# Optimization experiments

Hardware: AMD Instinct MI355X
Metric: run time of the kernel (lower is better)

## Reference

```python
import jax, jax.numpy as jnp
import numpy as np

N, C, DIM, K = 1024, 8, 128, 3
LBP_LOOPS = 10
DAMP = 0.5


def setup_inputs() -> dict:
    key = jax.random.key(0)
    ks = jax.random.split(key, 6)
    return {
        "E": jax.random.normal(ks[0], (N, C, DIM), dtype=jnp.float32),   # candidate entity embeddings e_{i,c}
        "F": jax.random.normal(ks[1], (N, DIM), dtype=jnp.float32),      # mention reps f(m_i) (f_m_c output)
        "Fc": jax.random.normal(ks[2], (N, DIM), dtype=jnp.float32),     # context reps f(c_i)
        "B": jax.random.normal(ks[3], (DIM,), dtype=jnp.float32),        # diagonal of B
        "R": jax.random.normal(ks[4], (K, DIM), dtype=jnp.float32),      # diagonals of R[k]
        "D": jax.random.normal(ks[5], (K, DIM), dtype=jnp.float32),      # diagonals of D[k]
    }


def reference(E, F, Fc, B, R, D):
    n, c, d = E.shape
    # psi[i, ci] = e_{i,ci}^T diag(B) f(c_i)
    psi = jnp.einsum('icd,d,id->ic', E, B, Fc)
    # a[i,j,k] = softmax_k( f_i^T diag(D[k]) f_j / sqrt(d) )   (RelNorm Z)
    logits = jnp.einsum('id,kd,jd->ijk', F, D, F) / jnp.sqrt(jnp.asarray(d, E.dtype))
    a = jax.nn.softmax(logits, axis=-1)
    # phi[i,j,ci,cj] = sum_k a[i,j,k] * e_{i,ci}^T diag(R[k]) e_{j,cj}
    Rw = jnp.einsum('ijk,kd->ijd', a, R)                 # [n, n, d]
    phi = jnp.einsum('icd,ijd,jed->ijce', E, Rw, E)      # [n, n, C, C]

    def lbp_step(mbar, _):
        # mbar[src, dst, cand_of_dst]
        incoming = mbar.sum(axis=0)                                 # [i, ci]
        excl = incoming[:, None, :] - jnp.transpose(mbar, (1, 0, 2))  # [i, j, ci] = sum_{k != j} mbar[k,i,ci]
        score = psi[:, None, :, None] + excl[:, :, :, None] + phi   # [i, j, ci, cj]
        msg = score.max(axis=2)                                     # max over ci -> [i, j, cj]
        new = jnp.log(DAMP * jax.nn.softmax(msg, axis=-1) + (1.0 - DAMP) * jnp.exp(mbar))
        return new, None

    mbar0 = jnp.zeros((n, n, c), dtype=E.dtype)
    mbar, _ = jax.lax.scan(lbp_step, mbar0, None, length=LBP_LOOPS)

    # ubar[i,c] = softmax_c( psi[i,c] + sum_{k != i} mbar[k,i,c] )
    self_msg = mbar[jnp.arange(n), jnp.arange(n)]        # [n, C]
    u = psi + mbar.sum(axis=0) - self_msg
    return jax.nn.softmax(u, axis=-1)
```

## Files before the change

kernel.cpp:

```cpp
#include <hip/hip_runtime.h>
#include <math.h>

#define N 1024
#define C 8
#define DIM 128
#define K 3
#define LBP_LOOPS 10
#define DAMP 0.5f

#define TI 16
#define TJ 16
#define DCH 32
#define ESTR 260
#define FSTR 132
#define SR 136
#define NT 64
#define NTILE 2080

typedef float v4f __attribute__((ext_vector_type(4)));

__device__ __forceinline__ int tri_base(int t) { return t * NT - (t * (t - 1)) / 2; }
__device__ __forceinline__ void tri_decode(int b, int& ti, int& tj) {
    int t = (int)((2.f * NT + 1.f - sqrtf((2.f * NT + 1.f) * (2.f * NT + 1.f) - 8.f * (float)b)) * 0.5f);
    t = min(max(t, 0), NT - 1);
    while (tri_base(t) > b) --t;
    while (tri_base(t + 1) <= b) ++t;
    ti = t; tj = t + (b - tri_base(t));
}

__device__ __forceinline__ size_t tri_idx(int i, int j) {
    return (size_t)i * N - (((size_t)i * (i - 1)) >> 1) + (size_t)(j - i);
}

__global__ void psi_kernel(const float* __restrict__ E, const float* __restrict__ Fc,
                           const float* __restrict__ B, float* __restrict__ psi) {
    int x = blockIdx.x * blockDim.x + threadIdx.x;
    if (x >= N * C) return;
    int i = x / C;
    const float* e = E + (size_t)x * DIM;
    const float* fc = Fc + (size_t)i * DIM;
    float s = 0.f;
#pragma unroll 8
    for (int d = 0; d < DIM; ++d) s = fmaf(e[d] * B[d], fc[d], s);
    psi[x] = s;
}


__global__ __launch_bounds__(256, 2) void phi_i16_sym_kernel(
    const float* __restrict__ E, const float* __restrict__ F,
    const float* __restrict__ R, const float* __restrict__ D,
    short* __restrict__ phiQ, float* __restrict__ pscale)
{
    __shared__ __align__(16) float sU[2 * TI * ESTR];
    int ti, tj;
    tri_decode(blockIdx.x, ti, tj);
    int i0 = ti * 16, j0 = tj * 16;
    int tid = threadIdx.x;
    int il = tid >> 4, jl = tid & 15;

    float* sFi = sU;
    float* sFj = sU + TI * FSTR;
    float* sEi = sU;
    float* sEj = sU + TI * ESTR;

    {
        const v4f* F4 = (const v4f*)F;
        for (int t = tid; t < TI * DIM / 4; t += 256) {
            int r = t >> 5, d4 = t & 31;
            *(v4f*)&sFi[r * FSTR + d4 * 4] = F4[(size_t)(i0 + r) * (DIM / 4) + d4];
            *(v4f*)&sFj[r * FSTR + d4 * 4] = F4[(size_t)(j0 + r) * (DIM / 4) + d4];
        }
    }
    __syncthreads();

    v4f lga0 = {0.f,0.f,0.f,0.f}, lga1 = lga0, lga2 = lga0;
    {
        const v4f* D4 = (const v4f*)D;
#pragma unroll 8
        for (int d4 = 0; d4 < DIM / 4; ++d4) {
            v4f fi = *(const v4f*)&sFi[il * FSTR + d4 * 4];
            v4f fj = *(const v4f*)&sFj[jl * FSTR + d4 * 4];
            v4f ff = fi * fj;
            lga0 += ff * D4[d4];
            lga1 += ff * D4[DIM / 4 + d4];
            lga2 += ff * D4[2 * DIM / 4 + d4];
        }
    }
    float lg0 = lga0.x + lga0.y + lga0.z + lga0.w;
    float lg1 = lga1.x + lga1.y + lga1.z + lga1.w;
    float lg2 = lga2.x + lga2.y + lga2.z + lga2.w;
    const float scale = 0.088388347648318447f;
    lg0 *= scale; lg1 *= scale; lg2 *= scale;
    float mx = fmaxf(fmaxf(lg0, lg1), lg2);
    float e0 = __expf(lg0 - mx), e1 = __expf(lg1 - mx), e2 = __expf(lg2 - mx);
    float inv = 1.f / (e0 + e1 + e2);
    float a0 = e0 * inv, a1 = e1 * inv, a2 = e2 * inv;

    float acc[C][C];
#pragma unroll
    for (int ci = 0; ci < C; ++ci)
#pragma unroll
        for (int cj = 0; cj < C; ++cj) acc[ci][cj] = 0.f;

    const v4f* R4 = (const v4f*)R;
    for (int d0 = 0; d0 < DIM; d0 += DCH) {
        __syncthreads();
        for (int t = tid; t < TI * C * DCH; t += 256) {
            int loc = t >> 8, ci = (t >> 5) & 7, d = t & 31;
            sEi[loc * ESTR + ci * DCH + d] = E[((size_t)(i0 + loc) * C + ci) * DIM + d0 + d];
            sEj[loc * ESTR + ci * DCH + d] = E[((size_t)(j0 + loc) * C + ci) * DIM + d0 + d];
        }
        __syncthreads();
#pragma unroll
        for (int d4 = 0; d4 < DCH / 4; ++d4) {
            int rq = (d0 >> 2) + d4;
            v4f rw = R4[rq] * a0 + R4[(DIM >> 2) + rq] * a1 + R4[(DIM >> 1) + rq] * a2;
            v4f ei[C];
#pragma unroll
            for (int ci = 0; ci < C; ++ci)
                ei[ci] = *(const v4f*)&sEi[il * ESTR + ci * DCH + d4 * 4] * rw;
#pragma unroll
            for (int cj = 0; cj < C; ++cj) {
                v4f ej = *(const v4f*)&sEj[jl * ESTR + cj * DCH + d4 * 4];
#pragma unroll
                for (int ci = 0; ci < C; ++ci) {
                    acc[ci][cj] = fmaf(ei[ci].x, ej.x, acc[ci][cj]);
                    acc[ci][cj] = fmaf(ei[ci].y, ej.y, acc[ci][cj]);
                    acc[ci][cj] = fmaf(ei[ci].z, ej.z, acc[ci][cj]);
                    acc[ci][cj] = fmaf(ei[ci].w, ej.w, acc[ci][cj]);
                }
            }
        }
    }

    int i = i0 + il, j = j0 + jl;
    if (i > j) return;

    float amax = 0.f;
#pragma unroll
    for (int ci = 0; ci < C; ++ci)
#pragma unroll
        for (int cj = 0; cj < C; ++cj) amax = fmaxf(amax, fabsf(acc[ci][cj]));
    float qs = (amax > 0.f) ? (32767.0f / amax) : 1.0f;

    size_t tri = tri_idx(i, j);
    pscale[tri] = (amax > 0.f) ? (amax / 32767.0f) : 0.f;

    int4* out = (int4*)(phiQ + tri * (C * C));
#pragma unroll
    for (int ci = 0; ci < C; ++ci) {
        int q[C];
#pragma unroll
        for (int cj = 0; cj < C; ++cj) q[cj] = (int)rintf(acc[ci][cj] * qs);
        int4 v;
        v.x = (q[0] & 0xFFFF) | (q[1] << 16);
        v.y = (q[2] & 0xFFFF) | (q[3] << 16);
        v.z = (q[4] & 0xFFFF) | (q[5] << 16);
        v.w = (q[6] & 0xFFFF) | (q[7] << 16);
        out[ci] = v;
    }
}


__device__ __forceinline__ void damp_calc(const float msg[C], const float mpv[C], float o[C]) {
    float mx = msg[0];
#pragma unroll
    for (int c = 1; c < C; ++c) mx = fmaxf(mx, msg[c]);
    float e[C], s = 0.f;
#pragma unroll
    for (int c = 0; c < C; ++c) { e[c] = __expf(msg[c] - mx); s += e[c]; }
    float inv = DAMP / s;
#pragma unroll
    for (int c = 0; c < C; ++c)
        o[c] = __logf(fmaf(e[c], inv, (1.f - DAMP) * __expf(mpv[c])));
}

template <bool FIRST>
__global__ __launch_bounds__(256) void lbp_tile(
    const short* __restrict__ phiQ, const float* __restrict__ pscale,
    const float* __restrict__ mprev, float* __restrict__ mnext,
    const float* __restrict__ incpsi, float* __restrict__ partInc)
{
    int ti, tj;
    tri_decode(blockIdx.x, ti, tj);
    bool diag = (ti == tj);
    __shared__ __align__(16) float sA[16 * SR];
    __shared__ __align__(16) float sB[16 * SR];
    __shared__ float sInc[256];
    int tid = threadIdx.x;
    int i0 = ti * 16, j0 = tj * 16;

    if (!FIRST) {
        const float4* __restrict__ src = (const float4*)mprev;
        for (int t = tid; t < 512; t += 256) {
            int row = t >> 5, rem = t & 31;
            float4 v = src[((size_t)(i0 + row) * N + j0) * 2 + rem];
            *(float4*)&sA[row * SR + rem * 4] = v;
        }
        if (!diag) {
            for (int t = tid; t < 512; t += 256) {
                int row = t >> 5, rem = t & 31;
                float4 v = src[((size_t)(j0 + row) * N + i0) * 2 + rem];
                *(float4*)&sB[row * SR + rem * 4] = v;
            }
        }
    }
    if (tid < 128) sInc[tid] = incpsi[i0 * C + tid];
    else sInc[tid] = incpsi[j0 * C + (tid - 128)];
    __syncthreads();

    int il = tid >> 4, jl = tid & 15;
    int i = i0 + il, j = j0 + jl;
    bool active = (!diag) || (jl >= il);
    bool dopair = active && (j > i);
    const float* sBB = diag ? sA : sB;

    float out_ij[C], out_ji[C];
    if (active) {
        float mij[C], mji[C], sci[C], scj[C];
#pragma unroll
        for (int c = 0; c < C; ++c) {
            mij[c] = FIRST ? 0.f : sA[il * SR + jl * 8 + c];
            mji[c] = FIRST ? 0.f : sBB[jl * SR + il * 8 + c];
            sci[c] = sInc[il * 8 + c] - mji[c];
            scj[c] = sInc[128 + jl * 8 + c] - mij[c];
        }

        size_t tri = tri_idx(i, j);
        float s = pscale[tri];
        float msg_ij[C], msg_ji[C];
#pragma unroll
        for (int c = 0; c < C; ++c) { msg_ij[c] = -1e30f; msg_ji[c] = -1e30f; }

        const int4* p4 = (const int4*)(phiQ + tri * (C * C));
#pragma unroll
        for (int ci = 0; ci < C; ++ci) {
            int4 v = p4[ci];
            float ph[C];
            ph[0] = (float)((int)(short)(v.x & 0xFFFF)) * s;
            ph[1] = (float)(v.x >> 16) * s;
            ph[2] = (float)((int)(short)(v.y & 0xFFFF)) * s;
            ph[3] = (float)(v.y >> 16) * s;
            ph[4] = (float)((int)(short)(v.z & 0xFFFF)) * s;
            ph[5] = (float)(v.z >> 16) * s;
            ph[6] = (float)((int)(short)(v.w & 0xFFFF)) * s;
            ph[7] = (float)(v.w >> 16) * s;
#pragma unroll
            for (int cj = 0; cj < C; ++cj) {
                msg_ij[cj] = fmaxf(msg_ij[cj], sci[ci] + ph[cj]);
                msg_ji[ci] = fmaxf(msg_ji[ci], scj[cj] + ph[cj]);
            }
        }
        damp_calc(msg_ij, mij, out_ij);
        if (dopair) damp_calc(msg_ji, mji, out_ji);
    }
    __syncthreads();

    if (active) {
#pragma unroll
        for (int c = 0; c < C; ++c) sA[il * SR + jl * 8 + c] = out_ij[c];
        if (dopair) {
            if (diag) {
#pragma unroll
                for (int c = 0; c < C; ++c) sA[jl * SR + il * 8 + c] = out_ji[c];
            } else {
#pragma unroll
                for (int c = 0; c < C; ++c) sB[jl * SR + il * 8 + c] = out_ji[c];
            }
        }
    }
    __syncthreads();

    {
        float4* __restrict__ dst = (float4*)mnext;
        for (int t = tid; t < 512; t += 256) {
            int row = t >> 5, rem = t & 31;
            dst[((size_t)(i0 + row) * N + j0) * 2 + rem] = *(const float4*)&sA[row * SR + rem * 4];
        }
        if (!diag) {
            for (int t = tid; t < 512; t += 256) {
                int row = t >> 5, rem = t & 31;
                dst[((size_t)(j0 + row) * N + i0) * 2 + rem] = *(const float4*)&sB[row * SR + rem * 4];
            }
        }
    }

    if (tid < 128) {
        int l = tid >> 3, c = tid & 7;
        float s = 0.f;
#pragma unroll
        for (int k = 0; k < 16; ++k) s += sA[k * SR + l * 8 + c];
        partInc[(size_t)ti * (N * C) + (j0 + l) * C + c] = s;
    } else if (!diag) {
        int t2 = tid - 128;
        int l = t2 >> 3, c = t2 & 7;
        float s = 0.f;
#pragma unroll
        for (int k = 0; k < 16; ++k) s += sB[k * SR + l * 8 + c];
        partInc[(size_t)tj * (N * C) + (i0 + l) * C + c] = s;
    }
}

__global__ void incfin_kernel(const float* __restrict__ partInc, const float* __restrict__ psi,
                              float* __restrict__ incpsi) {
    int x = blockIdx.x * 256 + threadIdx.x;
    if (x >= N * C) return;
    float s = psi[x];
#pragma unroll 8
    for (int g = 0; g < NT; ++g) s += partInc[(size_t)g * (N * C) + x];
    incpsi[x] = s;
}

__global__ void final_kernel(const float* __restrict__ incpsi, const float* __restrict__ mbar,
                             float* __restrict__ out) {
    int i = blockIdx.x * blockDim.x + threadIdx.x;
    if (i >= N) return;
    float u[C];
    float mx = -1e30f;
#pragma unroll
    for (int c = 0; c < C; ++c) {
        u[c] = incpsi[i * C + c] - mbar[((size_t)i * N + i) * C + c];
        mx = fmaxf(mx, u[c]);
    }
    float s = 0.f;
#pragma unroll
    for (int c = 0; c < C; ++c) { u[c] = __expf(u[c] - mx); s += u[c]; }
    float inv = 1.f / s;
#pragma unroll
    for (int c = 0; c < C; ++c) out[i * C + c] = u[c] * inv;
}


extern "C" void kernel_launch(void* const* d_in, const int* in_sizes, int n_in,
                              void* d_out, int out_size, void* d_ws, size_t ws_size,
                              hipStream_t stream) {
    const float* E  = (const float*)d_in[0];
    const float* F  = (const float*)d_in[1];
    const float* Fc = (const float*)d_in[2];
    const float* B  = (const float*)d_in[3];
    const float* R  = (const float*)d_in[4];
    const float* D  = (const float*)d_in[5];
    float* out = (float*)d_out;

    const size_t NPAIR   = (size_t)N * (N + 1) / 2;
    const size_t PHI_SZ  = NPAIR * C * C * 2;
    const size_t PSC_SZ  = NPAIR * 4;
    const size_t MBAR    = (size_t)N * N * C * 4;
    const size_t PART_SZ = (size_t)NT * N * C * 4;

    char* p = (char*)d_ws;
    short* phiQ   = (short*)p;                     p += PHI_SZ;
    float* pscale = (float*)p;                     p += PSC_SZ;
    float* mbar0  = (float*)p;                     p += MBAR;
    float* mbar1  = (float*)p;                     p += MBAR;
    float* partInc= (float*)p;                     p += PART_SZ;
    float* psi    = (float*)p;                     p += (size_t)N * C * 4;
    float* incpsi = (float*)p;

    psi_kernel<<<dim3((N * C + 255) / 256), 256, 0, stream>>>(E, Fc, B, psi);
    phi_i16_sym_kernel<<<dim3(NTILE), 256, 0, stream>>>(E, F, R, D, phiQ, pscale);

    float* cur = mbar0;
    float* nxt = mbar1;
    lbp_tile<true><<<dim3(NTILE), 256, 0, stream>>>(phiQ, pscale, cur, nxt, psi, partInc);
    incfin_kernel<<<dim3((N * C + 255) / 256), 256, 0, stream>>>(partInc, psi, incpsi);
    { float* t = cur; cur = nxt; nxt = t; }
    for (int it = 1; it < LBP_LOOPS; ++it) {
        lbp_tile<false><<<dim3(NTILE), 256, 0, stream>>>(phiQ, pscale, cur, nxt, incpsi, partInc);
        incfin_kernel<<<dim3((N * C + 255) / 256), 256, 0, stream>>>(partInc, psi, incpsi);
        float* t = cur; cur = nxt; nxt = t;
    }
    final_kernel<<<dim3((N + 255) / 256), 256, 0, stream>>>(incpsi, cur, out);
}
```

Before: 476.9 us.

## Prefetch E chunks into registers with vectorized loads to overlap phi compute

```diff
diff --git a/kernel.cpp b/kernel.cpp
--- a/kernel.cpp
+++ b/kernel.cpp
@@ -11,8 +11,10 @@
 #define TI 16
 #define TJ 16
 #define DCH 32
+#define NCH (DIM / DCH)
 #define ESTR 260
 #define FSTR 132
+#define SIDE (TI * ESTR)
 #define SR 136
 #define NT 64
 #define NTILE 2080
@@ -51,20 +53,21 @@
     const float* __restrict__ R, const float* __restrict__ D,
     short* __restrict__ phiQ, float* __restrict__ pscale)
 {
-    __shared__ __align__(16) float sU[2 * TI * ESTR];
+    __shared__ __align__(16) float sU[2 * SIDE];
     int ti, tj;
     tri_decode(blockIdx.x, ti, tj);
     int i0 = ti * 16, j0 = tj * 16;
     int tid = threadIdx.x;
     int il = tid >> 4, jl = tid & 15;
 
-    float* sFi = sU;
-    float* sFj = sU + TI * FSTR;
-    float* sEi = sU;
-    float* sEj = sU + TI * ESTR;
+    const v4f* E4 = (const v4f*)E;
+    const v4f* F4 = (const v4f*)F;
+    const v4f* R4 = (const v4f*)R;
+    const v4f* D4 = (const v4f*)D;
 
     {
-        const v4f* F4 = (const v4f*)F;
+        float* sFi = sU;
+        float* sFj = sU + TI * FSTR;
         for (int t = tid; t < TI * DIM / 4; t += 256) {
             int r = t >> 5, d4 = t & 31;
             *(v4f*)&sFi[r * FSTR + d4 * 4] = F4[(size_t)(i0 + r) * (DIM / 4) + d4];
@@ -73,9 +76,32 @@
     }
     __syncthreads();
 
-    v4f lga0 = {0.f,0.f,0.f,0.f}, lga1 = lga0, lga2 = lga0;
+    int q0 = tid, q1 = tid + 256, q2 = tid + 512, q3 = tid + 768;
+    int loc0 = q0 >> 6, ci0 = (q0 >> 3) & 7, dd0 = q0 & 7;
+    int loc1 = q1 >> 6, ci1 = (q1 >> 3) & 7, dd1 = q1 & 7;
+    int loc2 = q2 >> 6, ci2 = (q2 >> 3) & 7, dd2 = q2 & 7;
+    int loc3 = q3 >> 6, ci3 = (q3 >> 3) & 7, dd3 = q3 & 7;
+    size_t gi0 = ((size_t)(i0 + loc0) * C + ci0) * (DIM / 4) + dd0;
+    size_t gi1 = ((size_t)(i0 + loc1) * C + ci1) * (DIM / 4) + dd1;
+    size_t gi2 = ((size_t)(i0 + loc2) * C + ci2) * (DIM / 4) + dd2;
+    size_t gi3 = ((size_t)(i0 + loc3) * C + ci3) * (DIM / 4) + dd3;
+    size_t gj0 = ((size_t)(j0 + loc0) * C + ci0) * (DIM / 4) + dd0;
+    size_t gj1 = ((size_t)(j0 + loc1) * C + ci1) * (DIM / 4) + dd1;
+    size_t gj2 = ((size_t)(j0 + loc2) * C + ci2) * (DIM / 4) + dd2;
+    size_t gj3 = ((size_t)(j0 + loc3) * C + ci3) * (DIM / 4) + dd3;
+    int l0 = loc0 * ESTR + ci0 * DCH + dd0 * 4;
+    int l1 = loc1 * ESTR + ci1 * DCH + dd1 * 4;
+    int l2 = loc2 * ESTR + ci2 * DCH + dd2 * 4;
+    int l3 = loc3 * ESTR + ci3 * DCH + dd3 * 4;
+
+    v4f rA0 = E4[gi0], rA1 = E4[gi1], rA2 = E4[gi2], rA3 = E4[gi3];
+    v4f rB0 = E4[gj0], rB1 = E4[gj1], rB2 = E4[gj2], rB3 = E4[gj3];
+
+    float a0, a1, a2;
     {
-        const v4f* D4 = (const v4f*)D;
+        const float* sFi = sU;
+        const float* sFj = sU + TI * FSTR;
+        v4f lga0 = {0.f,0.f,0.f,0.f}, lga1 = lga0, lga2 = lga0;
 #pragma unroll 8
         for (int d4 = 0; d4 < DIM / 4; ++d4) {
             v4f fi = *(const v4f*)&sFi[il * FSTR + d4 * 4];
@@ -85,16 +111,23 @@
             lga1 += ff * D4[DIM / 4 + d4];
             lga2 += ff * D4[2 * DIM / 4 + d4];
         }
-    }
-    float lg0 = lga0.x + lga0.y + lga0.z + lga0.w;
-    float lg1 = lga1.x + lga1.y + lga1.z + lga1.w;
-    float lg2 = lga2.x + lga2.y + lga2.z + lga2.w;
-    const float scale = 0.088388347648318447f;
-    lg0 *= scale; lg1 *= scale; lg2 *= scale;
-    float mx = fmaxf(fmaxf(lg0, lg1), lg2);
-    float e0 = __expf(lg0 - mx), e1 = __expf(lg1 - mx), e2 = __expf(lg2 - mx);
-    float inv = 1.f / (e0 + e1 + e2);
-    float a0 = e0 * inv, a1 = e1 * inv, a2 = e2 * inv;
+        float lg0 = lga0.x + lga0.y + lga0.z + lga0.w;
+        float lg1 = lga1.x + lga1.y + lga1.z + lga1.w;
+        float lg2 = lga2.x + lga2.y + lga2.z + lga2.w;
+        const float scale = 0.088388347648318447f;
+        lg0 *= scale; lg1 *= scale; lg2 *= scale;
+        float mx = fmaxf(fmaxf(lg0, lg1), lg2);
+        float e0 = __expf(lg0 - mx), e1 = __expf(lg1 - mx), e2 = __expf(lg2 - mx);
+        float inv = 1.f / (e0 + e1 + e2);
+        a0 = e0 * inv; a1 = e1 * inv; a2 = e2 * inv;
+    }
+    __syncthreads();
+
+    *(v4f*)&sU[l0] = rA0; *(v4f*)&sU[l1] = rA1;
+    *(v4f*)&sU[l2] = rA2; *(v4f*)&sU[l3] = rA3;
+    *(v4f*)&sU[SIDE + l0] = rB0; *(v4f*)&sU[SIDE + l1] = rB1;
+    *(v4f*)&sU[SIDE + l2] = rB2; *(v4f*)&sU[SIDE + l3] = rB3;
+    __syncthreads();
 
     float acc[C][C];
 #pragma unroll
@@ -102,26 +135,27 @@
 #pragma unroll
         for (int cj = 0; cj < C; ++cj) acc[ci][cj] = 0.f;
 
-    const v4f* R4 = (const v4f*)R;
-    for (int d0 = 0; d0 < DIM; d0 += DCH) {
-        __syncthreads();
-        for (int t = tid; t < TI * C * DCH; t += 256) {
-            int loc = t >> 8, ci = (t >> 5) & 7, d = t & 31;
-            sEi[loc * ESTR + ci * DCH + d] = E[((size_t)(i0 + loc) * C + ci) * DIM + d0 + d];
-            sEj[loc * ESTR + ci * DCH + d] = E[((size_t)(j0 + loc) * C + ci) * DIM + d0 + d];
-        }
-        __syncthreads();
+    for (int c = 0; c < NCH; ++c) {
+        if (c < NCH - 1) {
+            size_t off = (size_t)((c + 1) * (DCH / 4));
+            rA0 = E4[gi0 + off]; rA1 = E4[gi1 + off];
+            rA2 = E4[gi2 + off]; rA3 = E4[gi3 + off];
+            rB0 = E4[gj0 + off]; rB1 = E4[gj1 + off];
+            rB2 = E4[gj2 + off]; rB3 = E4[gj3 + off];
+        }
+        const float* bi = sU + il * ESTR;
+        const float* bj = sU + SIDE + jl * ESTR;
 #pragma unroll
         for (int d4 = 0; d4 < DCH / 4; ++d4) {
-            int rq = (d0 >> 2) + d4;
-            v4f rw = R4[rq] * a0 + R4[(DIM >> 2) + rq] * a1 + R4[(DIM >> 1) + rq] * a2;
+            int rq = c * (DCH / 4) + d4;
+            v4f rw = R4[rq] * a0 + R4[(DIM / 4) + rq] * a1 + R4[(DIM / 2) + rq] * a2;
             v4f ei[C];
 #pragma unroll
             for (int ci = 0; ci < C; ++ci)
-                ei[ci] = *(const v4f*)&sEi[il * ESTR + ci * DCH + d4 * 4] * rw;
+                ei[ci] = *(const v4f*)&bi[ci * DCH + d4 * 4] * rw;
 #pragma unroll
             for (int cj = 0; cj < C; ++cj) {
-                v4f ej = *(const v4f*)&sEj[jl * ESTR + cj * DCH + d4 * 4];
+                v4f ej = *(const v4f*)&bj[cj * DCH + d4 * 4];
 #pragma unroll
                 for (int ci = 0; ci < C; ++ci) {
                     acc[ci][cj] = fmaf(ei[ci].x, ej.x, acc[ci][cj]);
@@ -130,6 +164,14 @@
                     acc[ci][cj] = fmaf(ei[ci].w, ej.w, acc[ci][cj]);
                 }
             }
+        }
+        if (c < NCH - 1) {
+            __syncthreads();
+            *(v4f*)&sU[l0] = rA0; *(v4f*)&sU[l1] = rA1;
+            *(v4f*)&sU[l2] = rA2; *(v4f*)&sU[l3] = rA3;
+            *(v4f*)&sU[SIDE + l0] = rB0; *(v4f*)&sU[SIDE + l1] = rB1;
+            *(v4f*)&sU[SIDE + l2] = rB2; *(v4f*)&sU[SIDE + l3] = rB3;
+            __syncthreads();
         }
     }
 
```

Result: slower. 1.588 ms (+233.1%).

## Double-buffer E tiles via async global-to-LDS loads with XOR swizzle

Applied to the files above, without the earlier changes.

```diff
diff --git a/kernel.cpp b/kernel.cpp
--- a/kernel.cpp
+++ b/kernel.cpp
@@ -10,9 +10,9 @@
 
 #define TI 16
 #define TJ 16
-#define DCH 32
-#define ESTR 260
-#define FSTR 132
+#define DCH 16
+#define NCH (DIM / DCH)
+#define BUF_BYTES 16384
 #define SR 136
 #define NT 64
 #define NTILE 2080
@@ -30,6 +30,13 @@
 
 __device__ __forceinline__ size_t tri_idx(int i, int j) {
     return (size_t)i * N - (((size_t)i * (i - 1)) >> 1) + (size_t)(j - i);
+}
+
+__device__ __forceinline__ void dma16(const void* g, void* l) {
+    __builtin_amdgcn_global_load_lds(
+        (const __attribute__((address_space(1))) void*)g,
+        (__attribute__((address_space(3))) void*)(unsigned)(uintptr_t)l,
+        16, 0, 0);
 }
 
 __global__ void psi_kernel(const float* __restrict__ E, const float* __restrict__ Fc,
@@ -46,55 +53,85 @@
 }
 
 
-__global__ __launch_bounds__(256, 2) void phi_i16_sym_kernel(
+__global__ __launch_bounds__(256) void phi_i16_sym_kernel(
     const float* __restrict__ E, const float* __restrict__ F,
     const float* __restrict__ R, const float* __restrict__ D,
     short* __restrict__ phiQ, float* __restrict__ pscale)
 {
-    __shared__ __align__(16) float sU[2 * TI * ESTR];
+    __shared__ __align__(16) float sU[2 * BUF_BYTES / 4];
     int ti, tj;
     tri_decode(blockIdx.x, ti, tj);
     int i0 = ti * 16, j0 = tj * 16;
     int tid = threadIdx.x;
     int il = tid >> 4, jl = tid & 15;
-
-    float* sFi = sU;
-    float* sFj = sU + TI * FSTR;
-    float* sEi = sU;
-    float* sEj = sU + TI * ESTR;
+    int lane = tid & 63, w = tid >> 6;
+    int xi = il & 7, xj = jl & 7;
+
+    const v4f* E4 = (const v4f*)E;
+    const v4f* F4 = (const v4f*)F;
+    const v4f* R4 = (const v4f*)R;
+    const v4f* D4 = (const v4f*)D;
+
+    int segbase = w * 2;
+    int e4i[2], e4j[2];
+#pragma unroll
+    for (int s = 0; s < 2; ++s) {
+        int q16 = (segbase + s) * 64 + lane;
+        int loc = q16 >> 5;
+        int phys = q16 & 31;
+        int logical = (phys & 24) | ((phys ^ loc) & 7);
+        int ci = logical >> 2, d4 = logical & 3;
+        e4i[s] = ((i0 + loc) * C + ci) * (DIM / 4) + d4;
+        e4j[s] = ((j0 + loc) * C + ci) * (DIM / 4) + d4;
+    }
 
     {
-        const v4f* F4 = (const v4f*)F;
-        for (int t = tid; t < TI * DIM / 4; t += 256) {
-            int r = t >> 5, d4 = t & 31;
-            *(v4f*)&sFi[r * FSTR + d4 * 4] = F4[(size_t)(i0 + r) * (DIM / 4) + d4];
-            *(v4f*)&sFj[r * FSTR + d4 * 4] = F4[(size_t)(j0 + r) * (DIM / 4) + d4];
+        float* fb = sU + BUF_BYTES / 4;
+        for (int t = tid; t < 1024; t += 256) {
+            int side = t >> 9;
+            int r = (t >> 5) & 15;
+            int dr = t & 31;
+            int phys = (dr & 24) | ((dr ^ r) & 7);
+            int row = (side ? j0 : i0) + r;
+            *(v4f*)(fb + side * 2048 + r * 128 + phys * 4) = F4[(size_t)row * (DIM / 4) + dr];
+        }
+    }
+    {
+        char* b0 = (char*)sU;
+#pragma unroll
+        for (int s = 0; s < 2; ++s) {
+            dma16(E4 + e4i[s], b0 + (segbase + s) * 1024);
+            dma16(E4 + e4j[s], b0 + 8192 + (segbase + s) * 1024);
         }
     }
     __syncthreads();
 
-    v4f lga0 = {0.f,0.f,0.f,0.f}, lga1 = lga0, lga2 = lga0;
+    float a0, a1, a2;
     {
-        const v4f* D4 = (const v4f*)D;
+        const float* fb = sU + BUF_BYTES / 4;
+        v4f lga0 = {0.f,0.f,0.f,0.f}, lga1 = lga0, lga2 = lga0;
 #pragma unroll 8
         for (int d4 = 0; d4 < DIM / 4; ++d4) {
-            v4f fi = *(const v4f*)&sFi[il * FSTR + d4 * 4];
-            v4f fj = *(const v4f*)&sFj[jl * FSTR + d4 * 4];
+            int pI = (d4 & 24) | ((d4 ^ xi) & 7);
+            int pJ = (d4 & 24) | ((d4 ^ xj) & 7);
+            v4f fi = *(const v4f*)(fb + il * 128 + pI * 4);
+            v4f fj = *(const v4f*)(fb + 2048 + jl * 128 + pJ * 4);
             v4f ff = fi * fj;
             lga0 += ff * D4[d4];
             lga1 += ff * D4[DIM / 4 + d4];
             lga2 += ff * D4[2 * DIM / 4 + d4];
         }
-    }
-    float lg0 = lga0.x + lga0.y + lga0.z + lga0.w;
-    float lg1 = lga1.x + lga1.y + lga1.z + lga1.w;
-    float lg2 = lga2.x + lga2.y + lga2.z + lga2.w;
-    const float scale = 0.088388347648318447f;
-    lg0 *= scale; lg1 *= scale; lg2 *= scale;
-    float mx = fmaxf(fmaxf(lg0, lg1), lg2);
-    float e0 = __expf(lg0 - mx), e1 = __expf(lg1 - mx), e2 = __expf(lg2 - mx);
-    float inv = 1.f / (e0 + e1 + e2);
-    float a0 = e0 * inv, a1 = e1 * inv, a2 = e2 * inv;
+        float lg0 = lga0.x + lga0.y + lga0.z + lga0.w;
+        float lg1 = lga1.x + lga1.y + lga1.z + lga1.w;
+        float lg2 = lga2.x + lga2.y + lga2.z + lga2.w;
+        const float scale = 0.088388347648318447f;
+        lg0 *= scale; lg1 *= scale; lg2 *= scale;
+        float mx = fmaxf(fmaxf(lg0, lg1), lg2);
+        float e0 = __expf(lg0 - mx), e1 = __expf(lg1 - mx), e2 = __expf(lg2 - mx);
+        float inv = 1.f / (e0 + e1 + e2);
+        a0 = e0 * inv; a1 = e1 * inv; a2 = e2 * inv;
+    }
+    __syncthreads();
 
     float acc[C][C];
 #pragma unroll
@@ -102,26 +139,33 @@
 #pragma unroll
         for (int cj = 0; cj < C; ++cj) acc[ci][cj] = 0.f;
 
-    const v4f* R4 = (const v4f*)R;
-    for (int d0 = 0; d0 < DIM; d0 += DCH) {
-        __syncthreads();
-        for (int t = tid; t < TI * C * DCH; t += 256) {
-            int loc = t >> 8, ci = (t >> 5) & 7, d = t & 31;
-            sEi[loc * ESTR + ci * DCH + d] = E[((size_t)(i0 + loc) * C + ci) * DIM + d0 + d];
-            sEj[loc * ESTR + ci * DCH + d] = E[((size_t)(j0 + loc) * C + ci) * DIM + d0 + d];
-        }
-        __syncthreads();
+    for (int c = 0; c < NCH; ++c) {
+        if (c < NCH - 1) {
+            char* bn = (char*)sU + (1 - (c & 1)) * BUF_BYTES;
+            int cf4 = (c + 1) * (DCH / 4);
+#pragma unroll
+            for (int s = 0; s < 2; ++s) {
+                dma16(E4 + e4i[s] + cf4, bn + (segbase + s) * 1024);
+                dma16(E4 + e4j[s] + cf4, bn + 8192 + (segbase + s) * 1024);
+            }
+        }
+        const char* bp = (const char*)sU + (c & 1) * BUF_BYTES;
+        const char* bi = bp + (il << 9);
+        const char* bj = bp + 8192 + (jl << 9);
 #pragma unroll
         for (int d4 = 0; d4 < DCH / 4; ++d4) {
-            int rq = (d0 >> 2) + d4;
-            v4f rw = R4[rq] * a0 + R4[(DIM >> 2) + rq] * a1 + R4[(DIM >> 1) + rq] * a2;
+            int rq = c * (DCH / 4) + d4;
+            v4f rw = R4[rq] * a0 + R4[(DIM / 4) + rq] * a1 + R4[(DIM / 2) + rq] * a2;
             v4f ei[C];
 #pragma unroll
-            for (int ci = 0; ci < C; ++ci)
-                ei[ci] = *(const v4f*)&sEi[il * ESTR + ci * DCH + d4 * 4] * rw;
+            for (int ci = 0; ci < C; ++ci) {
+                int pI = ((ci & 6) << 2) | ((((ci & 1) << 2) | d4) ^ xi);
+                ei[ci] = *(const v4f*)(bi + (pI << 4)) * rw;
+            }
 #pragma unroll
             for (int cj = 0; cj < C; ++cj) {
-                v4f ej = *(const v4f*)&sEj[jl * ESTR + cj * DCH + d4 * 4];
+                int pJ = ((cj & 6) << 2) | ((((cj & 1) << 2) | d4) ^ xj);
+                v4f ej = *(const v4f*)(bj + (pJ << 4));
 #pragma unroll
                 for (int ci = 0; ci < C; ++ci) {
                     acc[ci][cj] = fmaf(ei[ci].x, ej.x, acc[ci][cj]);
@@ -131,6 +175,7 @@
                 }
             }
         }
+        if (c < NCH - 1) __syncthreads();
     }
 
     int i = i0 + il, j = j0 + jl;
```

New measurement: 537.7 us. +12.7%, slower.
